# Kernel tuning notes

Hardware: AMD Instinct MI355X
Metric: run time of the kernel (lower is better)

## Reference

```python
import jax, jax.numpy as jnp
import numpy as np
from jax import lax

B, T, D, NH = 8, 2048, 128, 4
HD = D // NH
EPS = 1e-5


def _ln(x, g, b):
    m = x.mean(-1, keepdims=True)
    v = ((x - m) ** 2).mean(-1, keepdims=True)
    return (x - m) / jnp.sqrt(v + EPS) * g + b


def _gelu(x):  # exact (erf) GELU, matching torch nn.GELU default
    return jax.nn.gelu(x, approximate=False)


def _forward(lob_feat, trade_feat, has_trade,
             ei_w, ei_b, ei_g, ei_beta, decay,
             in_proj_w, in_proj_b, out_proj_w, out_proj_b,
             cn_g, cn_b,
             lob_w, lob_b, lob_g, lob_beta,
             tr_w, tr_b, tr_g, tr_beta,
             of_w, of_b, of_g, of_beta):
    # event impact: Linear -> LayerNorm -> Tanh, gated by has_trade
    impact = jnp.tanh(_ln(trade_feat @ ei_w.T + ei_b, ei_g, ei_beta))
    impact = impact * has_trade[..., None]              # [B,T,D]

    # diagonal linear recurrence: state_t = sigmoid(decay) * state_{t-1} + impact_t
    d = jax.nn.sigmoid(decay)                           # [D]

    def step(s, x):
        s = d * s + x
        return s, s

    _, states = lax.scan(step, jnp.zeros_like(impact[:, 0]),
                         jnp.swapaxes(impact, 0, 1))    # [T,B,D]
    state_seq = jnp.swapaxes(states, 0, 1)              # [B,T,D]

    # fusion MLPs (dropout is identity in eval)
    lob_enh = _gelu(_ln(jnp.concatenate([lob_feat, state_seq], -1) @ lob_w.T + lob_b,
                        lob_g, lob_beta))
    trade_enh = _gelu(_ln(jnp.concatenate([trade_feat, state_seq], -1) @ tr_w.T + tr_b,
                          tr_g, tr_beta))

    # torch nn.MultiheadAttention (batch_first): q=lob_enh, k=v=trade_enh
    wq, wk, wv = in_proj_w[:D], in_proj_w[D:2 * D], in_proj_w[2 * D:]
    bq, bk, bv = in_proj_b[:D], in_proj_b[D:2 * D], in_proj_b[2 * D:]
    q = (lob_enh @ wq.T + bq).reshape(B, T, NH, HD)
    k = (trade_enh @ wk.T + bk).reshape(B, T, NH, HD)
    v = (trade_enh @ wv.T + bv).reshape(B, T, NH, HD)
    scores = jnp.einsum('bqhd,bkhd->bhqk', q, k) / jnp.sqrt(jnp.float32(HD))
    attn = jax.nn.softmax(scores, axis=-1)
    ctx = jnp.einsum('bhqk,bkhd->bqhd', attn, v).reshape(B, T, D)
    fused_attn = ctx @ out_proj_w.T + out_proj_b

    fused = _ln(lob_enh + fused_attn, cn_g, cn_b)
    output = _gelu(_ln(jnp.concatenate([fused, trade_enh], -1) @ of_w.T + of_b,
                       of_g, of_beta))
    return output


def setup_inputs() -> dict:
    key = jax.random.key(0)
    ks = jax.random.split(key, 20)
    s1 = 1.0 / np.sqrt(D)
    s2 = 1.0 / np.sqrt(2 * D)
    return {
        'lob_feat': jax.random.normal(ks[0], (B, T, D), jnp.float32),
        'trade_feat': jax.random.normal(ks[1], (B, T, D), jnp.float32),
        'has_trade': (jax.random.uniform(ks[2], (B, T)) < 0.5).astype(jnp.float32),
        'ei_w': jax.random.normal(ks[3], (D, D), jnp.float32) * s1,
        'ei_b': jnp.zeros((D,), jnp.float32),
        'ei_g': jnp.ones((D,), jnp.float32),
        'ei_beta': jnp.zeros((D,), jnp.float32),
        'decay': jnp.ones((D,), jnp.float32) * 0.9,
        'in_proj_w': jax.random.normal(ks[4], (3 * D, D), jnp.float32) * s1,
        'in_proj_b': jnp.zeros((3 * D,), jnp.float32),
        'out_proj_w': jax.random.normal(ks[5], (D, D), jnp.float32) * s1,
        'out_proj_b': jnp.zeros((D,), jnp.float32),
        'cn_g': jnp.ones((D,), jnp.float32),
        'cn_b': jnp.zeros((D,), jnp.float32),
        'lob_w': jax.random.normal(ks[6], (D, 2 * D), jnp.float32) * s2,
        'lob_b': jnp.zeros((D,), jnp.float32),
        'lob_g': jnp.ones((D,), jnp.float32),
        'lob_beta': jnp.zeros((D,), jnp.float32),
        'tr_w': jax.random.normal(ks[7], (D, 2 * D), jnp.float32) * s2,
        'tr_b': jnp.zeros((D,), jnp.float32),
        'tr_g': jnp.ones((D,), jnp.float32),
        'tr_beta': jnp.zeros((D,), jnp.float32),
        'of_w': jax.random.normal(ks[8], (D, 2 * D), jnp.float32) * s2,
        'of_b': jnp.zeros((D,), jnp.float32),
        'of_g': jnp.ones((D,), jnp.float32),
        'of_beta': jnp.zeros((D,), jnp.float32),
    }


def reference(lob_feat, trade_feat, has_trade,
              ei_w, ei_b, ei_g, ei_beta, decay,
              in_proj_w, in_proj_b, out_proj_w, out_proj_b,
              cn_g, cn_b,
              lob_w, lob_b, lob_g, lob_beta,
              tr_w, tr_b, tr_g, tr_beta,
              of_w, of_b, of_g, of_beta):
    return _forward(lob_feat, trade_feat, has_trade,
                    ei_w, ei_b, ei_g, ei_beta, decay,
                    in_proj_w, in_proj_b, out_proj_w, out_proj_b,
                    cn_g, cn_b,
                    lob_w, lob_b, lob_g, lob_beta,
                    tr_w, tr_b, tr_g, tr_beta,
                    of_w, of_b, of_g, of_beta)
```

## Files before the change

kernel.cpp:

```cpp
#include <hip/hip_runtime.h>
#include <math.h>


#define T_  2048

typedef short bf16x8 __attribute__((ext_vector_type(8)));
typedef float f32x4  __attribute__((ext_vector_type(4)));
typedef unsigned short ushort_t;

__device__ __forceinline__ float sigm(float x) { return 1.0f / (1.0f + __expf(-x)); }

__device__ __forceinline__ unsigned short f2bf(float x) {
    union { float f; unsigned u; } v; v.f = x;
    unsigned r = v.u + 0x7FFFu + ((v.u >> 16) & 1u);
    return (unsigned short)(r >> 16);
}
__device__ __forceinline__ float bf2f(ushort_t u) {
    union { unsigned u; float f; } v; v.u = ((unsigned)u) << 16; return v.f;
}

__device__ __forceinline__ float gelu_f(float x) {
    const float e = exp2f(fmaf(0.044715f * x, x * x, x) * -2.3022083f);
    return x * __builtin_amdgcn_rcpf(1.0f + e);
}
__device__ __forceinline__ float tanh_f(float y) {
    const float e = exp2f(y * 2.8853900818f);
    return 1.0f - 2.0f * __builtin_amdgcn_rcpf(e + 1.0f);
}

__global__ __launch_bounds__(256) void prep_kernel(
    const float* __restrict__ lob, const float* __restrict__ trade,
    const float* __restrict__ eiw, const float* __restrict__ ipw,
    const float* __restrict__ opw, const float* __restrict__ lobw,
    const float* __restrict__ trw, const float* __restrict__ ofw,
    ushort_t* __restrict__ pool)
{
    const size_t i8 = ((size_t)blockIdx.x * 256 + threadIdx.x) * 8;
    const float* src; size_t off;
    if      (i8 < 2097152) { src = lob;   off = 0; }
    else if (i8 < 4194304) { src = trade; off = 2097152; }
    else if (i8 < 4210688) { src = eiw;   off = 4194304; }
    else if (i8 < 4259840) { src = ipw;   off = 4210688; }
    else if (i8 < 4276224) { src = opw;   off = 4259840; }
    else if (i8 < 4308992) { src = lobw;  off = 4276224; }
    else if (i8 < 4341760) { src = trw;   off = 4308992; }
    else                   { src = ofw;   off = 4341760; }
    const float4 a = *(const float4*)(src + (i8 - off));
    const float4 b = *(const float4*)(src + (i8 - off) + 4);
    bf16x8 o;
    o[0] = (short)f2bf(a.x); o[1] = (short)f2bf(a.y);
    o[2] = (short)f2bf(a.z); o[3] = (short)f2bf(a.w);
    o[4] = (short)f2bf(b.x); o[5] = (short)f2bf(b.y);
    o[6] = (short)f2bf(b.z); o[7] = (short)f2bf(b.w);
    *(bf16x8*)(pool + i8) = o;
}

__global__ __launch_bounds__(256) void gemm_ei(
    const ushort_t* __restrict__ Xb0, const ushort_t* __restrict__ Wb,
    const float* __restrict__ bias, const float* __restrict__ gamma,
    const float* __restrict__ beta, const float* __restrict__ extra,
    ushort_t* __restrict__ outb)
{
    __shared__ float red[32][2][2];
    const int tid = threadIdx.x, wid = tid >> 6, lane = tid & 63;
    const int c2 = lane & 15, g = lane >> 4;
    const int rowblk = wid >> 1, chf = wid & 1, cb0 = chf * 4;
    const int R0 = blockIdx.x * 32 + rowblk * 16;

    f32x4 acc[4] = {};
#pragma unroll
    for (int ch = 0; ch < 4; ch++) {
        const bf16x8 a = *(const bf16x8*)(Xb0 + (size_t)(R0 + c2) * 128 + ch * 32 + g * 8);
#pragma unroll
        for (int j = 0; j < 4; j++) {
            const bf16x8 b = *(const bf16x8*)(Wb + (size_t)((cb0 + j) * 16 + c2) * 128 + ch * 32 + g * 8);
            acc[j] = __builtin_amdgcn_mfma_f32_16x16x32_bf16(a, b, acc[j], 0, 0, 0);
        }
    }
    float gm[4], bt[4];
#pragma unroll
    for (int j = 0; j < 4; j++) {
        const int col = (cb0 + j) * 16 + c2;
        const float bb = bias[col];
        gm[j] = gamma[col]; bt[j] = beta[col];
#pragma unroll
        for (int r = 0; r < 4; r++) acc[j][r] += bb;
    }
#pragma unroll
    for (int r = 0; r < 4; r++) {
        float s = 0.f, ss = 0.f;
#pragma unroll
        for (int j = 0; j < 4; j++) { const float v = acc[j][r]; s += v; ss = fmaf(v, v, ss); }
#pragma unroll
        for (int o = 8; o; o >>= 1) { s += __shfl_xor(s, o); ss += __shfl_xor(ss, o); }
        if (c2 == 0) {
            red[rowblk * 16 + 4 * g + r][chf][0] = s;
            red[rowblk * 16 + 4 * g + r][chf][1] = ss;
        }
    }
    __syncthreads();
#pragma unroll
    for (int r = 0; r < 4; r++) {
        const int lr = rowblk * 16 + 4 * g + r;
        const float S  = red[lr][0][0] + red[lr][1][0];
        const float SS = red[lr][0][1] + red[lr][1][1];
        const float mean = S * (1.0f / 128.0f);
        float var = SS * (1.0f / 128.0f) - mean * mean;
        var = fmaxf(var, 0.0f);
        const float rstd = rsqrtf(var + 1e-5f);
        const int R = blockIdx.x * 32 + lr;
        const float ext = extra[R];
#pragma unroll
        for (int j = 0; j < 4; j++) {
            const float y = (acc[j][r] - mean) * rstd * gm[j] + bt[j];
            outb[(size_t)R * 128 + (cb0 + j) * 16 + c2] = f2bf(tanh_f(y) * ext);
        }
    }
}

__global__ __launch_bounds__(256) void enh_qkv(
    const ushort_t* __restrict__ lobb, const ushort_t* __restrict__ trab,
    const ushort_t* __restrict__ stab,
    const ushort_t* __restrict__ lobw, const ushort_t* __restrict__ trw,
    const ushort_t* __restrict__ ipw, const float* __restrict__ ipb,
    const float* __restrict__ lob_b, const float* __restrict__ lob_g,
    const float* __restrict__ lob_beta,
    const float* __restrict__ tr_b, const float* __restrict__ tr_g,
    const float* __restrict__ tr_beta,
    float* __restrict__ lobe_f, ushort_t* __restrict__ tre_bf,
    ushort_t* __restrict__ qo, ushort_t* __restrict__ ko, ushort_t* __restrict__ vo)
{
    __shared__ ushort_t lob_t[32][136];
    __shared__ ushort_t tre_t[32][136];
    __shared__ ushort_t vls[128][36];
    __shared__ float red[32][2][4];
    const int tid = threadIdx.x, wid = tid >> 6, lane = tid & 63;
    const int c2 = lane & 15, g = lane >> 4;
    const int rowblk = wid >> 1, chf = wid & 1, cb0 = chf * 4;
    const int RB = blockIdx.x * 32;
    const int R0 = RB + rowblk * 16;

    f32x4 aL[4] = {}, aT[4] = {};
#pragma unroll
    for (int ch = 0; ch < 8; ch++) {
        const int kk = (ch & 3) * 32;
        bf16x8 xl, xt;
        if (ch < 4) {
            xl = *(const bf16x8*)(lobb + (size_t)(R0 + c2) * 128 + kk + g * 8);
            xt = *(const bf16x8*)(trab + (size_t)(R0 + c2) * 128 + kk + g * 8);
        } else {
            xl = *(const bf16x8*)(stab + (size_t)(R0 + c2) * 128 + kk + g * 8);
            xt = xl;
        }
#pragma unroll
        for (int j = 0; j < 4; j++) {
            const size_t wo = (size_t)((cb0 + j) * 16 + c2) * 256 + ch * 32 + g * 8;
            aL[j] = __builtin_amdgcn_mfma_f32_16x16x32_bf16(xl, *(const bf16x8*)(lobw + wo), aL[j], 0, 0, 0);
            aT[j] = __builtin_amdgcn_mfma_f32_16x16x32_bf16(xt, *(const bf16x8*)(trw + wo), aT[j], 0, 0, 0);
        }
    }
#pragma unroll
    for (int j = 0; j < 4; j++) {
        const int col = (cb0 + j) * 16 + c2;
        const float bL = lob_b[col], bT = tr_b[col];
#pragma unroll
        for (int r = 0; r < 4; r++) { aL[j][r] += bL; aT[j][r] += bT; }
    }
#pragma unroll
    for (int r = 0; r < 4; r++) {
        float sL = 0.f, ssL = 0.f, sT = 0.f, ssT = 0.f;
#pragma unroll
        for (int j = 0; j < 4; j++) {
            const float vL = aL[j][r], vT = aT[j][r];
            sL += vL; ssL = fmaf(vL, vL, ssL);
            sT += vT; ssT = fmaf(vT, vT, ssT);
        }
#pragma unroll
        for (int o = 8; o; o >>= 1) {
            sL += __shfl_xor(sL, o); ssL += __shfl_xor(ssL, o);
            sT += __shfl_xor(sT, o); ssT += __shfl_xor(ssT, o);
        }
        if (c2 == 0) {
            float* rd = red[rowblk * 16 + 4 * g + r][chf];
            rd[0] = sL; rd[1] = ssL; rd[2] = sT; rd[3] = ssT;
        }
    }
    __syncthreads();
#pragma unroll
    for (int r = 0; r < 4; r++) {
        const int lr = rowblk * 16 + 4 * g + r;
        const int R = RB + lr;
        const float SL  = red[lr][0][0] + red[lr][1][0];
        const float SSL = red[lr][0][1] + red[lr][1][1];
        const float ST  = red[lr][0][2] + red[lr][1][2];
        const float SST = red[lr][0][3] + red[lr][1][3];
        const float mL = SL * (1.0f / 128.0f), mT = ST * (1.0f / 128.0f);
        const float rL = rsqrtf(fmaxf(SSL * (1.0f / 128.0f) - mL * mL, 0.0f) + 1e-5f);
        const float rT = rsqrtf(fmaxf(SST * (1.0f / 128.0f) - mT * mT, 0.0f) + 1e-5f);
#pragma unroll
        for (int j = 0; j < 4; j++) {
            const int col = (cb0 + j) * 16 + c2;
            const float yL = gelu_f((aL[j][r] - mL) * rL * lob_g[col] + lob_beta[col]);
            const float yT = gelu_f((aT[j][r] - mT) * rT * tr_g[col] + tr_beta[col]);
            lobe_f[(size_t)R * 128 + col] = yL;
            lob_t[lr][col] = f2bf(yL);
            const ushort_t tb = f2bf(yT);
            tre_bf[(size_t)R * 128 + col] = tb;
            tre_t[lr][col] = tb;
        }
    }
    __syncthreads();

    const float qscale = 0.17677669529663687f * 1.4426950408889634f;
#pragma unroll
    for (int which = 0; which < 3; which++) {
        const ushort_t (*src)[136] = (which == 0) ? lob_t : tre_t;
        const ushort_t* Wp = ipw + (size_t)which * 16384;
        f32x4 pa[4] = {};
#pragma unroll
        for (int ch = 0; ch < 4; ch++) {
            const bf16x8 a = *(const bf16x8*)&src[rowblk * 16 + c2][ch * 32 + g * 8];
#pragma unroll
            for (int j = 0; j < 4; j++) {
                const bf16x8 b = *(const bf16x8*)(Wp + (size_t)((cb0 + j) * 16 + c2) * 128 + ch * 32 + g * 8);
                pa[j] = __builtin_amdgcn_mfma_f32_16x16x32_bf16(a, b, pa[j], 0, 0, 0);
            }
        }
        if (which < 2) {
            ushort_t* dst = (which == 0) ? qo : ko;
            const float sc = (which == 0) ? qscale : 1.0f;
#pragma unroll
            for (int j = 0; j < 4; j++) {
                const int col = (cb0 + j) * 16 + c2;
                const float bb = ipb[which * 128 + col];
                const int h = col >> 5, hd = col & 31;
#pragma unroll
                for (int r = 0; r < 4; r++) {
                    const int R = R0 + 4 * g + r;
                    const int b = R >> 11, t = R & 2047;
                    dst[(((size_t)b * 4 + h) * 2048 + t) * 32 + hd] = f2bf((pa[j][r] + bb) * sc);
                }
            }
        } else {
#pragma unroll
            for (int j = 0; j < 4; j++) {
                const int col = (cb0 + j) * 16 + c2;
                const float bb = ipb[256 + col];
#pragma unroll
                for (int r = 0; r < 4; r++)
                    vls[col][rowblk * 16 + 4 * g + r] = f2bf(pa[j][r] + bb);
            }
        }
    }
    __syncthreads();
    {
        const int col = tid >> 1, hf = tid & 1;
        const int h = col >> 5, hd = col & 31;
        const int b = RB >> 11;
        unsigned w[8];
#pragma unroll
        for (int e = 0; e < 8; e++) {
            const int p0 = hf * 16 + 2 * e;
            const int g2 = p0 >> 3, j2 = p0 & 7;
            const int lk = 4 * g2 + j2 + (j2 >= 4 ? 12 : 0);
            w[e] = (unsigned)vls[col][lk] | ((unsigned)vls[col][lk + 1] << 16);
        }
        ushort_t* dst = vo + (((size_t)b * 4 + h) * 32 + hd) * 2048 + (RB & 2047) + hf * 16;
        *(uint4*)dst       = *(const uint4*)&w[0];
        *(uint4*)(dst + 8) = *(const uint4*)&w[4];
    }
}

__global__ __launch_bounds__(256) void attn_kernel(
    const ushort_t* __restrict__ q, const ushort_t* __restrict__ k,
    const ushort_t* __restrict__ vtg, ushort_t* __restrict__ ctx)
{
    __shared__ ushort_t ks[2][64][40];
    __shared__ ushort_t vt[2][32][72];
    const int tid = threadIdx.x, wid = tid >> 6, lane = tid & 63;
    const int c = lane & 15, g = lane >> 4;
    const int qt = blockIdx.x, bh = blockIdx.y, b = bh >> 2, h = bh & 3;
    const ushort_t* kb_ = k   + (size_t)bh * 65536;
    const ushort_t* vb_ = vtg + (size_t)bh * 65536;

    const bf16x8 qf = *(const bf16x8*)(q + ((size_t)bh * 2048 + qt * 64 + wid * 16 + c) * 32 + g * 8);

    float m_i = 8.0f, rs = 0.0f;
    f32x4 acc[2] = {};

    const int srow = tid >> 2, ssg = tid & 3;
    const int vd = tid >> 3, vkg = tid & 7;

    {
        const bf16x8 kk8 = *(const bf16x8*)(kb_ + (size_t)srow * 32 + ssg * 8);
        const bf16x8 vv8 = *(const bf16x8*)(vb_ + (size_t)vd * 2048 + vkg * 8);
        *(bf16x8*)&ks[0][srow][ssg * 8] = kk8;
        *(bf16x8*)&vt[0][vd][vkg * 8] = vv8;
    }
    __syncthreads();

    for (int kt = 0; kt < 32; kt++) {
        const int cur = kt & 1;
        bf16x8 kk8, vv8;
        if (kt + 1 < 32) {
            kk8 = *(const bf16x8*)(kb_ + ((size_t)(kt + 1) * 64 + srow) * 32 + ssg * 8);
            vv8 = *(const bf16x8*)(vb_ + (size_t)vd * 2048 + (kt + 1) * 64 + vkg * 8);
        }

        f32x4 s[4];
        __builtin_amdgcn_s_setprio(1);
#pragma unroll
        for (int kb2 = 0; kb2 < 4; kb2++) {
            const bf16x8 kf = *(const bf16x8*)&ks[cur][kb2 * 16 + c][g * 8];
            f32x4 z = {};
            s[kb2] = __builtin_amdgcn_mfma_f32_16x16x32_bf16(kf, qf, z, 0, 0, 0);
        }
        __builtin_amdgcn_s_setprio(0);

        float lm = s[0][0];
#pragma unroll
        for (int kb2 = 0; kb2 < 4; kb2++)
#pragma unroll
            for (int r = 0; r < 4; r++) lm = fmaxf(lm, s[kb2][r]);
        if (__any(lm > m_i + 40.0f)) {
            float tm = lm;
            tm = fmaxf(tm, __shfl_xor(tm, 16));
            tm = fmaxf(tm, __shfl_xor(tm, 32));
            const float mn = fmaxf(m_i, tm);
            const float al = exp2f(m_i - mn);
            rs *= al;
#pragma unroll
            for (int nb = 0; nb < 2; nb++)
#pragma unroll
                for (int r = 0; r < 4; r++) acc[nb][r] *= al;
            m_i = mn;
        }

#pragma unroll
        for (int kb2 = 0; kb2 < 4; kb2++)
#pragma unroll
            for (int r = 0; r < 4; r++) s[kb2][r] = exp2f(s[kb2][r] - m_i);
        rs += ((s[0][0] + s[0][1]) + (s[0][2] + s[0][3]))
            + ((s[1][0] + s[1][1]) + (s[1][2] + s[1][3]))
            + ((s[2][0] + s[2][1]) + (s[2][2] + s[2][3]))
            + ((s[3][0] + s[3][1]) + (s[3][2] + s[3][3]));
        union { unsigned u[4]; bf16x8 v; } pf0, pf1;
        asm("v_cvt_pk_bf16_f32 %0, %1, %2" : "=v"(pf0.u[0]) : "v"(s[0][0]), "v"(s[0][1]));
        asm("v_cvt_pk_bf16_f32 %0, %1, %2" : "=v"(pf0.u[1]) : "v"(s[0][2]), "v"(s[0][3]));
        asm("v_cvt_pk_bf16_f32 %0, %1, %2" : "=v"(pf0.u[2]) : "v"(s[1][0]), "v"(s[1][1]));
        asm("v_cvt_pk_bf16_f32 %0, %1, %2" : "=v"(pf0.u[3]) : "v"(s[1][2]), "v"(s[1][3]));
        asm("v_cvt_pk_bf16_f32 %0, %1, %2" : "=v"(pf1.u[0]) : "v"(s[2][0]), "v"(s[2][1]));
        asm("v_cvt_pk_bf16_f32 %0, %1, %2" : "=v"(pf1.u[1]) : "v"(s[2][2]), "v"(s[2][3]));
        asm("v_cvt_pk_bf16_f32 %0, %1, %2" : "=v"(pf1.u[2]) : "v"(s[3][0]), "v"(s[3][1]));
        asm("v_cvt_pk_bf16_f32 %0, %1, %2" : "=v"(pf1.u[3]) : "v"(s[3][2]), "v"(s[3][3]));

        __builtin_amdgcn_s_setprio(1);
#pragma unroll
        for (int nb = 0; nb < 2; nb++) {
            const bf16x8 v0 = *(const bf16x8*)&vt[cur][nb * 16 + c][g * 8];
            const bf16x8 v1 = *(const bf16x8*)&vt[cur][nb * 16 + c][32 + g * 8];
            acc[nb] = __builtin_amdgcn_mfma_f32_16x16x32_bf16(v0, pf0.v, acc[nb], 0, 0, 0);
            acc[nb] = __builtin_amdgcn_mfma_f32_16x16x32_bf16(v1, pf1.v, acc[nb], 0, 0, 0);
        }
        __builtin_amdgcn_s_setprio(0);

        if (kt + 1 < 32) {
            *(bf16x8*)&ks[cur ^ 1][srow][ssg * 8] = kk8;
            *(bf16x8*)&vt[cur ^ 1][vd][vkg * 8] = vv8;
        }
        __syncthreads();
    }

    rs += __shfl_xor(rs, 16);
    rs += __shfl_xor(rs, 32);
    const float inv = __builtin_amdgcn_rcpf(rs);
    const int q_ = qt * 64 + wid * 16 + c;
    ushort_t* dst = ctx + ((size_t)(b * 2048 + q_)) * 128 + h * 32;
#pragma unroll
    for (int nb = 0; nb < 2; nb++) {
        unsigned w0, w1;
        const float a0 = acc[nb][0] * inv, a1 = acc[nb][1] * inv;
        const float a2 = acc[nb][2] * inv, a3 = acc[nb][3] * inv;
        asm("v_cvt_pk_bf16_f32 %0, %1, %2" : "=v"(w0) : "v"(a0), "v"(a1));
        asm("v_cvt_pk_bf16_f32 %0, %1, %2" : "=v"(w1) : "v"(a2), "v"(a3));
        uint2 wv; wv.x = w0; wv.y = w1;
        *(uint2*)(dst + nb * 16 + 4 * g) = wv;
    }
}

__global__ __launch_bounds__(256) void out_fuse(
    const ushort_t* __restrict__ ctxb, const ushort_t* __restrict__ treb,
    const ushort_t* __restrict__ opw, const float* __restrict__ opb,
    const float* __restrict__ cn_g, const float* __restrict__ cn_b,
    const ushort_t* __restrict__ ofw, const float* __restrict__ of_b,
    const float* __restrict__ of_g, const float* __restrict__ of_beta,
    const float* __restrict__ lobe_f, float* __restrict__ out)
{
    __shared__ ushort_t fus_t[32][136];
    __shared__ float red[32][2][2];
    const int tid = threadIdx.x, wid = tid >> 6, lane = tid & 63;
    const int c2 = lane & 15, g = lane >> 4;
    const int rowblk = wid >> 1, chf = wid & 1, cb0 = chf * 4;
    const int RB = blockIdx.x * 32;
    const int R0 = RB + rowblk * 16;

    f32x4 acc[4] = {};
#pragma unroll
    for (int ch = 0; ch < 4; ch++) {
        const bf16x8 a = *(const bf16x8*)(ctxb + (size_t)(R0 + c2) * 128 + ch * 32 + g * 8);
#pragma unroll
        for (int j = 0; j < 4; j++) {
            const bf16x8 b = *(const bf16x8*)(opw + (size_t)((cb0 + j) * 16 + c2) * 128 + ch * 32 + g * 8);
            acc[j] = __builtin_amdgcn_mfma_f32_16x16x32_bf16(a, b, acc[j], 0, 0, 0);
        }
    }
#pragma unroll
    for (int j = 0; j < 4; j++) {
        const int col = (cb0 + j) * 16 + c2;
        const float bb = opb[col];
#pragma unroll
        for (int r = 0; r < 4; r++)
            acc[j][r] += bb + lobe_f[(size_t)(R0 + 4 * g + r) * 128 + col];
    }
#pragma unroll
    for (int r = 0; r < 4; r++) {
        float s = 0.f, ss = 0.f;
#pragma unroll
        for (int j = 0; j < 4; j++) { const float v = acc[j][r]; s += v; ss = fmaf(v, v, ss); }
#pragma unroll
        for (int o = 8; o; o >>= 1) { s += __shfl_xor(s, o); ss += __shfl_xor(ss, o); }
        if (c2 == 0) {
            red[rowblk * 16 + 4 * g + r][chf][0] = s;
            red[rowblk * 16 + 4 * g + r][chf][1] = ss;
        }
    }
    __syncthreads();
#pragma unroll
    for (int r = 0; r < 4; r++) {
        const int lr = rowblk * 16 + 4 * g + r;
        const float S  = red[lr][0][0] + red[lr][1][0];
        const float SS = red[lr][0][1] + red[lr][1][1];
        const float mean = S * (1.0f / 128.0f);
        const float rstd = rsqrtf(fmaxf(SS * (1.0f / 128.0f) - mean * mean, 0.0f) + 1e-5f);
#pragma unroll
        for (int j = 0; j < 4; j++) {
            const int col = (cb0 + j) * 16 + c2;
            fus_t[lr][col] = f2bf((acc[j][r] - mean) * rstd * cn_g[col] + cn_b[col]);
        }
    }
    __syncthreads();

    f32x4 a2[4] = {};
#pragma unroll
    for (int ch = 0; ch < 8; ch++) {
        bf16x8 a;
        if (ch < 4) a = *(const bf16x8*)&fus_t[rowblk * 16 + c2][ch * 32 + g * 8];
        else        a = *(const bf16x8*)(treb + (size_t)(R0 + c2) * 128 + (ch - 4) * 32 + g * 8);
#pragma unroll
        for (int j = 0; j < 4; j++) {
            const bf16x8 b = *(const bf16x8*)(ofw + (size_t)((cb0 + j) * 16 + c2) * 256 + ch * 32 + g * 8);
            a2[j] = __builtin_amdgcn_mfma_f32_16x16x32_bf16(a, b, a2[j], 0, 0, 0);
        }
    }
#pragma unroll
    for (int j = 0; j < 4; j++) {
        const float bb = of_b[(cb0 + j) * 16 + c2];
#pragma unroll
        for (int r = 0; r < 4; r++) a2[j][r] += bb;
    }
#pragma unroll
    for (int r = 0; r < 4; r++) {
        float s = 0.f, ss = 0.f;
#pragma unroll
        for (int j = 0; j < 4; j++) { const float v = a2[j][r]; s += v; ss = fmaf(v, v, ss); }
#pragma unroll
        for (int o = 8; o; o >>= 1) { s += __shfl_xor(s, o); ss += __shfl_xor(ss, o); }
        if (c2 == 0) {
            red[rowblk * 16 + 4 * g + r][chf][0] = s;
            red[rowblk * 16 + 4 * g + r][chf][1] = ss;
        }
    }
    __syncthreads();
#pragma unroll
    for (int r = 0; r < 4; r++) {
        const int lr = rowblk * 16 + 4 * g + r;
        const float S  = red[lr][0][0] + red[lr][1][0];
        const float SS = red[lr][0][1] + red[lr][1][1];
        const float mean = S * (1.0f / 128.0f);
        const float rstd = rsqrtf(fmaxf(SS * (1.0f / 128.0f) - mean * mean, 0.0f) + 1e-5f);
        const int R = RB + lr;
#pragma unroll
        for (int j = 0; j < 4; j++) {
            const int col = (cb0 + j) * 16 + c2;
            const float y = (a2[j][r] - mean) * rstd * of_g[col] + of_beta[col];
            out[(size_t)R * 128 + col] = gelu_f(y);
        }
    }
}

__global__ void scan_ends_kernel(const ushort_t* __restrict__ imp,
                                 const float* __restrict__ decay,
                                 float* __restrict__ ends)
{
    const int c = threadIdx.x;
    const int ch = blockIdx.x, b = blockIdx.y;
    const float d = sigm(decay[c]);
    const size_t base = ((size_t)b * T_ + ch * 64) * 128 + c;
    float s = 0.0f;
#pragma unroll 4
    for (int tl = 0; tl < 64; tl++)
        s = fmaf(d, s, bf2f(imp[base + (size_t)tl * 128]));
    ends[((size_t)b * 32 + ch) * 128 + c] = s;
}

__global__ void scan_carry_kernel(const float* __restrict__ ends,
                                  const float* __restrict__ decay,
                                  float* __restrict__ carry)
{
    const int c = threadIdx.x;
    const int b = blockIdx.x;
    const float d = sigm(decay[c]);
    float dl = d;
#pragma unroll
    for (int i = 0; i < 6; i++) dl *= dl;
    float e = 0.0f;
#pragma unroll
    for (int ch = 0; ch < 32; ch++) {
        carry[((size_t)b * 32 + ch) * 128 + c] = e;
        e = fmaf(dl, e, ends[((size_t)b * 32 + ch) * 128 + c]);
    }
}

__global__ void scan_fin_kernel(const ushort_t* __restrict__ imp,
                                const float* __restrict__ decay,
                                const float* __restrict__ carry,
                                ushort_t* __restrict__ stbf)
{
    const int c = threadIdx.x;
    const int ch = blockIdx.x, b = blockIdx.y;
    const float d = sigm(decay[c]);
    float s = carry[((size_t)b * 32 + ch) * 128 + c];
    const size_t base = ((size_t)b * T_ + ch * 64) * 128 + c;
#pragma unroll 4
    for (int tl = 0; tl < 64; tl++) {
        s = fmaf(d, s, bf2f(imp[base + (size_t)tl * 128]));
        stbf[base + (size_t)tl * 128] = f2bf(s);
    }
}

extern "C" void kernel_launch(void* const* d_in, const int* in_sizes, int n_in,
                              void* d_out, int out_size, void* d_ws, size_t ws_size,
                              hipStream_t stream)
{
    const float* lob_feat   = (const float*)d_in[0];
    const float* trade_feat = (const float*)d_in[1];
    const float* has_trade  = (const float*)d_in[2];
    const float* ei_w       = (const float*)d_in[3];
    const float* ei_b       = (const float*)d_in[4];
    const float* ei_g       = (const float*)d_in[5];
    const float* ei_beta    = (const float*)d_in[6];
    const float* decay      = (const float*)d_in[7];
    const float* in_proj_w  = (const float*)d_in[8];
    const float* in_proj_b  = (const float*)d_in[9];
    const float* out_proj_w = (const float*)d_in[10];
    const float* out_proj_b = (const float*)d_in[11];
    const float* cn_g       = (const float*)d_in[12];
    const float* cn_b       = (const float*)d_in[13];
    const float* lob_w      = (const float*)d_in[14];
    const float* lob_b      = (const float*)d_in[15];
    const float* lob_g      = (const float*)d_in[16];
    const float* lob_beta   = (const float*)d_in[17];
    const float* tr_w       = (const float*)d_in[18];
    const float* tr_b       = (const float*)d_in[19];
    const float* tr_g       = (const float*)d_in[20];
    const float* tr_beta    = (const float*)d_in[21];
    const float* of_w       = (const float*)d_in[22];
    const float* of_b       = (const float*)d_in[23];
    const float* of_g       = (const float*)d_in[24];
    const float* of_beta    = (const float*)d_in[25];

    char* W = (char*)d_ws;
    const size_t MB = 1u << 20;
    float*    lobe_f   = (float*)W;
    float*    carry    = (float*)(W + 8 * MB);
    float*    ends     = (float*)(W + 8 * MB + 256 * 1024);
    ushort_t* pool     = (ushort_t*)(W + 9 * MB);
    ushort_t* imp_bf   = (ushort_t*)(W + 18 * MB);
    ushort_t* state_bf = (ushort_t*)(W + 22 * MB);
    ushort_t* tre_bf   = (ushort_t*)(W + 26 * MB);
    ushort_t* q_bf     = (ushort_t*)(W + 30 * MB);
    ushort_t* k_bf     = (ushort_t*)(W + 34 * MB);
    ushort_t* vt_g     = (ushort_t*)(W + 38 * MB);
    ushort_t* ctx_bf   = (ushort_t*)(W + 42 * MB);

    ushort_t* lob_bf   = pool;
    ushort_t* trade_bf = pool + 2097152;
    ushort_t* eiw_bf   = pool + 4194304;
    ushort_t* ipw_bf   = pool + 4210688;
    ushort_t* opw_bf   = pool + 4259840;
    ushort_t* lobw_bf  = pool + 4276224;
    ushort_t* trw_bf   = pool + 4308992;
    ushort_t* ofw_bf   = pool + 4341760;

    const dim3 blk(256);

    prep_kernel<<<dim3(2136), blk, 0, stream>>>(lob_feat, trade_feat, ei_w, in_proj_w,
                                                out_proj_w, lob_w, tr_w, of_w, pool);
    gemm_ei<<<dim3(512), blk, 0, stream>>>(trade_bf, eiw_bf, ei_b, ei_g, ei_beta,
                                           has_trade, imp_bf);
    scan_ends_kernel<<<dim3(32, 8), dim3(128), 0, stream>>>(imp_bf, decay, ends);
    scan_carry_kernel<<<dim3(8), dim3(128), 0, stream>>>(ends, decay, carry);
    scan_fin_kernel<<<dim3(32, 8), dim3(128), 0, stream>>>(imp_bf, decay, carry, state_bf);
    enh_qkv<<<dim3(512), blk, 0, stream>>>(lob_bf, trade_bf, state_bf, lobw_bf, trw_bf,
                                           ipw_bf, in_proj_b, lob_b, lob_g, lob_beta,
                                           tr_b, tr_g, tr_beta, lobe_f, tre_bf,
                                           q_bf, k_bf, vt_g);
    attn_kernel<<<dim3(32, 32), blk, 0, stream>>>(q_bf, k_bf, vt_g, ctx_bf);
    out_fuse<<<dim3(512), blk, 0, stream>>>(ctx_bf, tre_bf, opw_bf, out_proj_b, cn_g, cn_b,
                                            ofw_bf, of_b, of_g, of_beta, lobe_f, (float*)d_out);
}
```

Measured before the change: 139.2 us.

## Split attention KV range in two, with a combine kernel and more query rows per wave

Each attention block now handles 128 query rows, 32 per wave, over half of the key range, so every K fragment loaded from shared memory feeds two query tiles. Partial outputs, row sums and maxima go to a workspace and a new combine kernel merges the two halves. Row sums are now computed with an MFMA against a ones vector, and the max-rescale path is skipped until scores exceed a threshold. The cost is an extra kernel launch, the partial-result round trip through global memory, and scattered 2-byte partial stores.

Result: slower. 144.2 us (+3.6%).

```diff
diff --git a/kernel.cpp b/kernel.cpp
--- a/kernel.cpp
+++ b/kernel.cpp
@@ -273,20 +273,31 @@
 
 __global__ __launch_bounds__(256) void attn_kernel(
     const ushort_t* __restrict__ q, const ushort_t* __restrict__ k,
-    const ushort_t* __restrict__ vtg, ushort_t* __restrict__ ctx)
+    const ushort_t* __restrict__ vtg,
+    ushort_t* __restrict__ part, float* __restrict__ rs_part,
+    float* __restrict__ m_part)
 {
     __shared__ ushort_t ks[2][64][40];
     __shared__ ushort_t vt[2][32][72];
     const int tid = threadIdx.x, wid = tid >> 6, lane = tid & 63;
     const int c = lane & 15, g = lane >> 4;
-    const int qt = blockIdx.x, bh = blockIdx.y, b = bh >> 2, h = bh & 3;
-    const ushort_t* kb_ = k   + (size_t)bh * 65536;
-    const ushort_t* vb_ = vtg + (size_t)bh * 65536;
-
-    const bf16x8 qf = *(const bf16x8*)(q + ((size_t)bh * 2048 + qt * 64 + wid * 16 + c) * 32 + g * 8);
-
-    float m_i = 8.0f, rs = 0.0f;
-    f32x4 acc[2] = {};
+    const int half = blockIdx.x & 1, qt = blockIdx.x >> 1;
+    const int bh = blockIdx.y;
+    const ushort_t* kb_ = k   + (size_t)bh * 65536 + (size_t)half * 1024 * 32;
+    const ushort_t* vb_ = vtg + (size_t)bh * 65536 + (size_t)half * 1024;
+    const int q0 = qt * 128 + wid * 32;
+
+    const ushort_t* qbase = q + ((size_t)bh * 2048 + q0) * 32;
+    const bf16x8 qf0 = *(const bf16x8*)(qbase + (size_t)c * 32 + g * 8);
+    const bf16x8 qf1 = *(const bf16x8*)(qbase + (size_t)(16 + c) * 32 + g * 8);
+
+    bf16x8 ones;
+#pragma unroll
+    for (int i = 0; i < 8; i++) ones[i] = (short)0x3F80;
+
+    float m0 = 0.0f, m1 = 0.0f;
+    f32x4 acc[2][2] = {};
+    f32x4 racc[2] = {};
 
     const int srow = tid >> 2, ssg = tid & 3;
     const int vd = tid >> 3, vkg = tid & 7;
@@ -299,93 +310,155 @@
     }
     __syncthreads();
 
-    for (int kt = 0; kt < 32; kt++) {
+    for (int kt = 0; kt < 16; kt++) {
         const int cur = kt & 1;
         bf16x8 kk8, vv8;
-        if (kt + 1 < 32) {
+        if (kt + 1 < 16) {
             kk8 = *(const bf16x8*)(kb_ + ((size_t)(kt + 1) * 64 + srow) * 32 + ssg * 8);
             vv8 = *(const bf16x8*)(vb_ + (size_t)vd * 2048 + (kt + 1) * 64 + vkg * 8);
         }
 
-        f32x4 s[4];
+        f32x4 s0[4], s1[4];
         __builtin_amdgcn_s_setprio(1);
 #pragma unroll
         for (int kb2 = 0; kb2 < 4; kb2++) {
             const bf16x8 kf = *(const bf16x8*)&ks[cur][kb2 * 16 + c][g * 8];
             f32x4 z = {};
-            s[kb2] = __builtin_amdgcn_mfma_f32_16x16x32_bf16(kf, qf, z, 0, 0, 0);
+            s0[kb2] = __builtin_amdgcn_mfma_f32_16x16x32_bf16(kf, qf0, z, 0, 0, 0);
+            s1[kb2] = __builtin_amdgcn_mfma_f32_16x16x32_bf16(kf, qf1, z, 0, 0, 0);
         }
         __builtin_amdgcn_s_setprio(0);
 
-        float lm = s[0][0];
-#pragma unroll
-        for (int kb2 = 0; kb2 < 4; kb2++)
-#pragma unroll
-            for (int r = 0; r < 4; r++) lm = fmaxf(lm, s[kb2][r]);
-        if (__any(lm > m_i + 40.0f)) {
-            float tm = lm;
-            tm = fmaxf(tm, __shfl_xor(tm, 16));
-            tm = fmaxf(tm, __shfl_xor(tm, 32));
-            const float mn = fmaxf(m_i, tm);
-            const float al = exp2f(m_i - mn);
-            rs *= al;
+        float lm = -1e30f;
+#pragma unroll
+        for (int kb2 = 0; kb2 < 4; kb2++) {
+            lm = fmaxf(lm, fmaxf(fmaxf(s0[kb2][0], s0[kb2][1]), fmaxf(s0[kb2][2], s0[kb2][3])));
+            lm = fmaxf(lm, fmaxf(fmaxf(s1[kb2][0], s1[kb2][1]), fmaxf(s1[kb2][2], s1[kb2][3])));
+        }
+        if (__any(lm > 80.0f || m0 != 0.0f || m1 != 0.0f)) {
+            float l0 = -1e30f, l1 = -1e30f;
+#pragma unroll
+            for (int kb2 = 0; kb2 < 4; kb2++) {
+#pragma unroll
+                for (int r = 0; r < 4; r++) { l0 = fmaxf(l0, s0[kb2][r]); l1 = fmaxf(l1, s1[kb2][r]); }
+            }
+            l0 = fmaxf(l0, __shfl_xor(l0, 16)); l0 = fmaxf(l0, __shfl_xor(l0, 32));
+            l1 = fmaxf(l1, __shfl_xor(l1, 16)); l1 = fmaxf(l1, __shfl_xor(l1, 32));
+            const float n0 = fmaxf(m0, l0), n1 = fmaxf(m1, l1);
+            const float a0 = exp2f(m0 - n0), a1 = exp2f(m1 - n1);
 #pragma unroll
             for (int nb = 0; nb < 2; nb++)
 #pragma unroll
-                for (int r = 0; r < 4; r++) acc[nb][r] *= al;
-            m_i = mn;
-        }
-
-#pragma unroll
-        for (int kb2 = 0; kb2 < 4; kb2++)
-#pragma unroll
-            for (int r = 0; r < 4; r++) s[kb2][r] = exp2f(s[kb2][r] - m_i);
-        rs += ((s[0][0] + s[0][1]) + (s[0][2] + s[0][3]))
-            + ((s[1][0] + s[1][1]) + (s[1][2] + s[1][3]))
-            + ((s[2][0] + s[2][1]) + (s[2][2] + s[2][3]))
-            + ((s[3][0] + s[3][1]) + (s[3][2] + s[3][3]));
-        union { unsigned u[4]; bf16x8 v; } pf0, pf1;
-        asm("v_cvt_pk_bf16_f32 %0, %1, %2" : "=v"(pf0.u[0]) : "v"(s[0][0]), "v"(s[0][1]));
-        asm("v_cvt_pk_bf16_f32 %0, %1, %2" : "=v"(pf0.u[1]) : "v"(s[0][2]), "v"(s[0][3]));
-        asm("v_cvt_pk_bf16_f32 %0, %1, %2" : "=v"(pf0.u[2]) : "v"(s[1][0]), "v"(s[1][1]));
-        asm("v_cvt_pk_bf16_f32 %0, %1, %2" : "=v"(pf0.u[3]) : "v"(s[1][2]), "v"(s[1][3]));
-        asm("v_cvt_pk_bf16_f32 %0, %1, %2" : "=v"(pf1.u[0]) : "v"(s[2][0]), "v"(s[2][1]));
-        asm("v_cvt_pk_bf16_f32 %0, %1, %2" : "=v"(pf1.u[1]) : "v"(s[2][2]), "v"(s[2][3]));
-        asm("v_cvt_pk_bf16_f32 %0, %1, %2" : "=v"(pf1.u[2]) : "v"(s[3][0]), "v"(s[3][1]));
-        asm("v_cvt_pk_bf16_f32 %0, %1, %2" : "=v"(pf1.u[3]) : "v"(s[3][2]), "v"(s[3][3]));
+                for (int r = 0; r < 4; r++) { acc[0][nb][r] *= a0; acc[1][nb][r] *= a1; }
+#pragma unroll
+            for (int r = 0; r < 4; r++) { racc[0][r] *= a0; racc[1][r] *= a1; }
+            m0 = n0; m1 = n1;
+#pragma unroll
+            for (int kb2 = 0; kb2 < 4; kb2++)
+#pragma unroll
+                for (int r = 0; r < 4; r++) {
+                    s0[kb2][r] = exp2f(s0[kb2][r] - m0);
+                    s1[kb2][r] = exp2f(s1[kb2][r] - m1);
+                }
+        } else {
+#pragma unroll
+            for (int kb2 = 0; kb2 < 4; kb2++)
+#pragma unroll
+                for (int r = 0; r < 4; r++) {
+                    s0[kb2][r] = exp2f(s0[kb2][r]);
+                    s1[kb2][r] = exp2f(s1[kb2][r]);
+                }
+        }
+
+        union { unsigned u[4]; bf16x8 v; } p0a, p0b, p1a, p1b;
+        asm("v_cvt_pk_bf16_f32 %0, %1, %2" : "=v"(p0a.u[0]) : "v"(s0[0][0]), "v"(s0[0][1]));
+        asm("v_cvt_pk_bf16_f32 %0, %1, %2" : "=v"(p0a.u[1]) : "v"(s0[0][2]), "v"(s0[0][3]));
+        asm("v_cvt_pk_bf16_f32 %0, %1, %2" : "=v"(p0a.u[2]) : "v"(s0[1][0]), "v"(s0[1][1]));
+        asm("v_cvt_pk_bf16_f32 %0, %1, %2" : "=v"(p0a.u[3]) : "v"(s0[1][2]), "v"(s0[1][3]));
+        asm("v_cvt_pk_bf16_f32 %0, %1, %2" : "=v"(p0b.u[0]) : "v"(s0[2][0]), "v"(s0[2][1]));
+        asm("v_cvt_pk_bf16_f32 %0, %1, %2" : "=v"(p0b.u[1]) : "v"(s0[2][2]), "v"(s0[2][3]));
+        asm("v_cvt_pk_bf16_f32 %0, %1, %2" : "=v"(p0b.u[2]) : "v"(s0[3][0]), "v"(s0[3][1]));
+        asm("v_cvt_pk_bf16_f32 %0, %1, %2" : "=v"(p0b.u[3]) : "v"(s0[3][2]), "v"(s0[3][3]));
+        asm("v_cvt_pk_bf16_f32 %0, %1, %2" : "=v"(p1a.u[0]) : "v"(s1[0][0]), "v"(s1[0][1]));
+        asm("v_cvt_pk_bf16_f32 %0, %1, %2" : "=v"(p1a.u[1]) : "v"(s1[0][2]), "v"(s1[0][3]));
+        asm("v_cvt_pk_bf16_f32 %0, %1, %2" : "=v"(p1a.u[2]) : "v"(s1[1][0]), "v"(s1[1][1]));
+        asm("v_cvt_pk_bf16_f32 %0, %1, %2" : "=v"(p1a.u[3]) : "v"(s1[1][2]), "v"(s1[1][3]));
+        asm("v_cvt_pk_bf16_f32 %0, %1, %2" : "=v"(p1b.u[0]) : "v"(s1[2][0]), "v"(s1[2][1]));
+        asm("v_cvt_pk_bf16_f32 %0, %1, %2" : "=v"(p1b.u[1]) : "v"(s1[2][2]), "v"(s1[2][3]));
+        asm("v_cvt_pk_bf16_f32 %0, %1, %2" : "=v"(p1b.u[2]) : "v"(s1[3][0]), "v"(s1[3][1]));
+        asm("v_cvt_pk_bf16_f32 %0, %1, %2" : "=v"(p1b.u[3]) : "v"(s1[3][2]), "v"(s1[3][3]));
 
         __builtin_amdgcn_s_setprio(1);
 #pragma unroll
         for (int nb = 0; nb < 2; nb++) {
             const bf16x8 v0 = *(const bf16x8*)&vt[cur][nb * 16 + c][g * 8];
             const bf16x8 v1 = *(const bf16x8*)&vt[cur][nb * 16 + c][32 + g * 8];
-            acc[nb] = __builtin_amdgcn_mfma_f32_16x16x32_bf16(v0, pf0.v, acc[nb], 0, 0, 0);
-            acc[nb] = __builtin_amdgcn_mfma_f32_16x16x32_bf16(v1, pf1.v, acc[nb], 0, 0, 0);
-        }
+            acc[0][nb] = __builtin_amdgcn_mfma_f32_16x16x32_bf16(v0, p0a.v, acc[0][nb], 0, 0, 0);
+            acc[0][nb] = __builtin_amdgcn_mfma_f32_16x16x32_bf16(v1, p0b.v, acc[0][nb], 0, 0, 0);
+            acc[1][nb] = __builtin_amdgcn_mfma_f32_16x16x32_bf16(v0, p1a.v, acc[1][nb], 0, 0, 0);
+            acc[1][nb] = __builtin_amdgcn_mfma_f32_16x16x32_bf16(v1, p1b.v, acc[1][nb], 0, 0, 0);
+        }
+        racc[0] = __builtin_amdgcn_mfma_f32_16x16x32_bf16(ones, p0a.v, racc[0], 0, 0, 0);
+        racc[0] = __builtin_amdgcn_mfma_f32_16x16x32_bf16(ones, p0b.v, racc[0], 0, 0, 0);
+        racc[1] = __builtin_amdgcn_mfma_f32_16x16x32_bf16(ones, p1a.v, racc[1], 0, 0, 0);
+        racc[1] = __builtin_amdgcn_mfma_f32_16x16x32_bf16(ones, p1b.v, racc[1], 0, 0, 0);
         __builtin_amdgcn_s_setprio(0);
 
-        if (kt + 1 < 32) {
+        if (kt + 1 < 16) {
             *(bf16x8*)&ks[cur ^ 1][srow][ssg * 8] = kk8;
             *(bf16x8*)&vt[cur ^ 1][vd][vkg * 8] = vv8;
         }
         __syncthreads();
     }
 
-    rs += __shfl_xor(rs, 16);
-    rs += __shfl_xor(rs, 32);
-    const float inv = __builtin_amdgcn_rcpf(rs);
-    const int q_ = qt * 64 + wid * 16 + c;
-    ushort_t* dst = ctx + ((size_t)(b * 2048 + q_)) * 128 + h * 32;
-#pragma unroll
-    for (int nb = 0; nb < 2; nb++) {
-        unsigned w0, w1;
-        const float a0 = acc[nb][0] * inv, a1 = acc[nb][1] * inv;
-        const float a2 = acc[nb][2] * inv, a3 = acc[nb][3] * inv;
-        asm("v_cvt_pk_bf16_f32 %0, %1, %2" : "=v"(w0) : "v"(a0), "v"(a1));
-        asm("v_cvt_pk_bf16_f32 %0, %1, %2" : "=v"(w1) : "v"(a2), "v"(a3));
-        uint2 wv; wv.x = w0; wv.y = w1;
-        *(uint2*)(dst + nb * 16 + 4 * g) = wv;
-    }
+    ushort_t* pb = part + (size_t)(half * 32 + bh) * 32 * 2048;
+#pragma unroll
+    for (int qf = 0; qf < 2; qf++) {
+        const int qrow = q0 + qf * 16 + c;
+#pragma unroll
+        for (int nb = 0; nb < 2; nb++)
+#pragma unroll
+            for (int r = 0; r < 4; r++)
+                pb[(size_t)(nb * 16 + 4 * g + r) * 2048 + qrow] = f2bf(acc[qf][nb][r]);
+    }
+    if (g == 0) {
+        float* rsp = rs_part + (size_t)(half * 32 + bh) * 2048;
+        float* mp  = m_part  + (size_t)(half * 32 + bh) * 2048;
+        rsp[q0 + c]      = racc[0][0];
+        rsp[q0 + 16 + c] = racc[1][0];
+        mp[q0 + c]       = m0;
+        mp[q0 + 16 + c]  = m1;
+    }
+}
+
+__global__ __launch_bounds__(256) void attn_combine(
+    const ushort_t* __restrict__ part, const float* __restrict__ rs_part,
+    const float* __restrict__ m_part, ushort_t* __restrict__ ctx)
+{
+    const int bh = blockIdx.y, tb = blockIdx.x;
+    const int b = bh >> 2, h = bh & 3;
+    const int t = tb * 128 + (threadIdx.x >> 1);
+    const int dh = threadIdx.x & 1;
+    const float mA = m_part[(size_t)bh * 2048 + t];
+    const float mB = m_part[(size_t)(32 + bh) * 2048 + t];
+    const float rA = rs_part[(size_t)bh * 2048 + t];
+    const float rB = rs_part[(size_t)(32 + bh) * 2048 + t];
+    const float M = fmaxf(mA, mB);
+    const float wA = exp2f(mA - M), wB = exp2f(mB - M);
+    const float inv = __builtin_amdgcn_rcpf(fmaf(rA, wA, rB * wB));
+    const ushort_t* pA = part + (size_t)bh * 32 * 2048;
+    const ushort_t* pB = part + (size_t)(32 + bh) * 32 * 2048;
+    ushort_t buf[16];
+#pragma unroll
+    for (int i = 0; i < 16; i++) {
+        const int d = dh * 16 + i;
+        const float v = fmaf(bf2f(pA[(size_t)d * 2048 + t]), wA,
+                             bf2f(pB[(size_t)d * 2048 + t]) * wB) * inv;
+        buf[i] = f2bf(v);
+    }
+    ushort_t* dst = ctx + ((size_t)(b * 2048 + t)) * 128 + h * 32 + dh * 16;
+    *(uint4*)dst = *(const uint4*)&buf[0];
+    *(uint4*)(dst + 8) = *(const uint4*)&buf[8];
 }
 
 __global__ __launch_bounds__(256) void out_fuse(
@@ -592,6 +665,9 @@
     ushort_t* k_bf     = (ushort_t*)(W + 34 * MB);
     ushort_t* vt_g     = (ushort_t*)(W + 38 * MB);
     ushort_t* ctx_bf   = (ushort_t*)(W + 42 * MB);
+    ushort_t* part     = (ushort_t*)(W + 46 * MB);
+    float*    rs_part  = (float*)(W + 54 * MB);
+    float*    m_part   = (float*)(W + 54 * MB + 512 * 1024);
 
     ushort_t* lob_bf   = pool;
     ushort_t* trade_bf = pool + 2097152;
@@ -615,7 +691,8 @@
                                            ipw_bf, in_proj_b, lob_b, lob_g, lob_beta,
                                            tr_b, tr_g, tr_beta, lobe_f, tre_bf,
                                            q_bf, k_bf, vt_g);
-    attn_kernel<<<dim3(32, 32), blk, 0, stream>>>(q_bf, k_bf, vt_g, ctx_bf);
+    attn_kernel<<<dim3(32, 32), blk, 0, stream>>>(q_bf, k_bf, vt_g, part, rs_part, m_part);
+    attn_combine<<<dim3(16, 32), blk, 0, stream>>>(part, rs_part, m_part, ctx_bf);
     out_fuse<<<dim3(512), blk, 0, stream>>>(ctx_bf, tre_bf, opw_bf, out_proj_b, cn_g, cn_b,
                                             ofw_bf, of_b, of_g, of_beta, lobe_f, (float*)d_out);
 }
```
